# Optimization experiments

Hardware: AMD Instinct MI355X
Metric: run time of the kernel (lower is better)

## Reference

```python
import jax, jax.numpy as jnp
import numpy as np

B, N, S = 4, 4096, 1024
C1, C2, CO, K = 128, 256, 128, 16
BN_EPS = 1e-5


def setup_inputs() -> dict:
    key = jax.random.key(0)
    ks = jax.random.split(key, 8)
    s = 0.05
    return {
        "xyz1": jax.random.normal(ks[0], (B, N, 3), jnp.float32),
        "xyz2": jax.random.normal(ks[1], (B, S, 3), jnp.float32),
        "points1": jax.random.normal(ks[2], (B, C1, N), jnp.float32),
        "points2": jax.random.normal(ks[3], (B, C2, S), jnp.float32),
        # fuse = ConvBNReLU1D(384 -> 128, k=1)
        "fuse_w": jax.random.normal(ks[4], (CO, C1 + C2), jnp.float32) * s,
        "fuse_b": jnp.zeros((CO,), jnp.float32),
        "fuse_gamma": jnp.ones((CO,), jnp.float32),
        "fuse_beta": jnp.zeros((CO,), jnp.float32),
        # LaplacianUnit conv1x1 (128 -> 128) + BN
        "lu_w": jax.random.normal(ks[5], (CO, CO), jnp.float32) * s,
        "lu_b": jnp.zeros((CO,), jnp.float32),
        "lu_gamma": jnp.ones((CO,), jnp.float32),
        "lu_beta": jnp.zeros((CO,), jnp.float32),
    }


def _sqdist(a, b):
    # a: [B,N,3], b: [B,M,3] -> [B,N,M] squared euclidean distance
    return ((a * a).sum(-1)[:, :, None] + (b * b).sum(-1)[:, None, :]
            - 2.0 * jnp.einsum("bnc,bmc->bnm", a, b))


def _batchnorm1d(x, gamma, beta):
    # x: [B,C,N], training-mode BN (batch statistics, biased variance)
    mean = x.mean(axis=(0, 2), keepdims=True)
    var = ((x - mean) ** 2).mean(axis=(0, 2), keepdims=True)
    xn = (x - mean) * jax.lax.rsqrt(var + BN_EPS)
    return xn * gamma[None, :, None] + beta[None, :, None]


def _gather_points(pts, idx):
    # pts: [B,M,C], idx: [B,N,k] int -> [B,N,k,C]
    return jax.vmap(lambda p, i: p[i])(pts, idx)


def _forward(xyz1, xyz2, points1, points2,
             fuse_w, fuse_b, fuse_gamma, fuse_beta,
             lu_w, lu_b, lu_gamma, lu_beta):
    p2 = jnp.swapaxes(points2, 1, 2)  # [B,S,C2]
    # --- 3-point interpolation (note: torch code uses topk default largest=True) ---
    dists = _sqdist(xyz1, xyz2)                    # [B,N,S]
    top_d, idx = jax.lax.top_k(dists, 3)           # largest, descending (faithful)
    dist_recip = 1.0 / (top_d + 1e-8)
    weight = dist_recip / dist_recip.sum(axis=2, keepdims=True)  # [B,N,3]
    interp = (_gather_points(p2, idx) * weight[..., None]).sum(axis=2)  # [B,N,C2]
    # --- concat skip + fuse conv1x1 + BN + ReLU ---
    new_pts = jnp.concatenate([jnp.swapaxes(points1, 1, 2), interp], axis=-1)  # [B,N,C1+C2]
    x = jnp.einsum("oc,bnc->bon", fuse_w, new_pts) + fuse_b[None, :, None]     # [B,CO,N]
    x = jax.nn.relu(_batchnorm1d(x, fuse_gamma, fuse_beta))
    # --- LaplacianUnit: KNN(k=16) neighbor-sum minus self ---
    d_self = _sqdist(xyz1, xyz1)                   # [B,N,N]
    _, knn_idx = jax.lax.top_k(-d_self, K)         # k smallest distances -> [B,N,K]
    xt = jnp.swapaxes(x, 1, 2)                     # [B,N,CO]
    nbr_sum = _gather_points(xt, knn_idx).sum(axis=2)  # [B,N,CO]
    dx = jnp.swapaxes(nbr_sum, 1, 2) - x           # [B,CO,N]
    h = jnp.einsum("oc,bcn->bon", lu_w, dx) + lu_b[None, :, None]
    h = _batchnorm1d(jax.nn.relu(h), lu_gamma, lu_beta)  # bn(relu(conv(dx))), faithful order
    return x + h


def reference(xyz1, xyz2, points1, points2,
              fuse_w, fuse_b, fuse_gamma, fuse_beta,
              lu_w, lu_b, lu_gamma, lu_beta):
    return _forward(xyz1, xyz2, points1, points2,
                    fuse_w, fuse_b, fuse_gamma, fuse_beta,
                    lu_w, lu_b, lu_gamma, lu_beta)
```

## Files before the change

kernel.cpp:

```cpp
#include <hip/hip_runtime.h>
#include <cfloat>

#define NB 4
#define NN 4096
#define NS 1024
#define NC1 128
#define NC2 256
#define NCO 128
#define NCC 384
#define NK 16
#define KCHUNK 2048
#define KCAP 96
#define KPAD 97


__device__ __forceinline__ float norm3_np(float x, float y, float z) {
  return __fadd_rn(__fadd_rn(__fmul_rn(x, x), __fmul_rn(y, y)), __fmul_rn(z, z));
}

__device__ __forceinline__ float sqdist_np(float nq, float ns,
                                           float qx, float qy, float qz,
                                           float sx, float sy, float sz) {
  float dot = __fadd_rn(__fadd_rn(__fmul_rn(qx, sx), __fmul_rn(qy, sy)),
                        __fmul_rn(qz, sz));
  return __fsub_rn(__fadd_rn(nq, ns), __fmul_rn(2.0f, dot));
}

__global__ void transpose_k(const float* __restrict__ in, float* __restrict__ out,
                            int rows_in, int cols_in, long in_bs, long out_bs, int out_rs) {
  __shared__ float tile[32][33];
  const int b = blockIdx.z;
  const int c0 = blockIdx.x * 32, r0 = blockIdx.y * 32;
  const float* ib = in + (long)b * in_bs;
  float* ob = out + (long)b * out_bs;
#pragma unroll
  for (int k = 0; k < 32; k += 8) {
    tile[threadIdx.y + k][threadIdx.x] =
        ib[(long)(r0 + threadIdx.y + k) * cols_in + c0 + threadIdx.x];
  }
  __syncthreads();
#pragma unroll
  for (int k = 0; k < 32; k += 8) {
    ob[(long)(c0 + threadIdx.y + k) * out_rs + (r0 + threadIdx.x)] =
        tile[threadIdx.x][threadIdx.y + k];
  }
}

__global__ __launch_bounds__(256) void interp_top3_k(const float* __restrict__ xyz1,
                                                     const float* __restrict__ xyz2,
                                                     float* __restrict__ wW,
                                                     int* __restrict__ wIdx) {
  __shared__ float sx[NS], sy[NS], sz[NS], sn[NS];
  __shared__ float md[256 * 3];
  __shared__ int mi[256 * 3];
  const int b = blockIdx.y;
  const int tid = threadIdx.x;
  for (int i = tid; i < NS; i += 256) {
    long base = ((long)b * NS + i) * 3;
    float x = xyz2[base], y = xyz2[base + 1], z = xyz2[base + 2];
    sx[i] = x; sy[i] = y; sz[i] = z;
    sn[i] = norm3_np(x, y, z);
  }
  __syncthreads();
  const int q = (blockIdx.x << 5) + (tid >> 3);
  const int lane = tid & 7;
  long qb = ((long)b * NN + q) * 3;
  const float qx = xyz1[qb], qy = xyz1[qb + 1], qz = xyz1[qb + 2];
  const float nq = norm3_np(qx, qy, qz);
  float bd[3] = {-FLT_MAX, -FLT_MAX, -FLT_MAX};
  int bi[3] = {0x7fffffff, 0x7fffffff, 0x7fffffff};
  for (int s = lane; s < NS; s += 8) {
    float d = sqdist_np(nq, sn[s], qx, qy, qz, sx[s], sy[s], sz[s]);
    float cd = d; int ci = s;
#pragma unroll
    for (int j = 0; j < 3; ++j) {
      bool gt = cd > bd[j];
      float f = fmaxf(cd, bd[j]);
      float bk = fminf(cd, bd[j]);
      int fi = gt ? ci : bi[j];
      int ki = gt ? bi[j] : ci;
      bd[j] = f; bi[j] = fi; cd = bk; ci = ki;
    }
  }
#pragma unroll
  for (int j = 0; j < 3; ++j) { md[tid * 3 + j] = bd[j]; mi[tid * 3 + j] = bi[j]; }
  __syncthreads();
  if (lane == 0) {
    int p0 = 0, p1 = 0, p2 = 0, p3 = 0, p4 = 0, p5 = 0, p6 = 0, p7 = 0;
    float od[3]; int oi[3];
#pragma unroll
    for (int j = 0; j < 3; ++j) {
      float bv = -FLT_MAX; int bidx = 0x7fffffff; int bl = 0;
#define ITOP_CAND(l, pl)                                                     \
      {                                                                      \
        float t = (pl < 3) ? md[(tid + l) * 3 + pl] : -FLT_MAX;              \
        int ti = (pl < 3) ? mi[(tid + l) * 3 + pl] : 0x7fffffff;             \
        if (t > bv || (t == bv && ti < bidx)) { bv = t; bidx = ti; bl = l; } \
      }
      ITOP_CAND(0, p0) ITOP_CAND(1, p1) ITOP_CAND(2, p2) ITOP_CAND(3, p3)
      ITOP_CAND(4, p4) ITOP_CAND(5, p5) ITOP_CAND(6, p6) ITOP_CAND(7, p7)
#undef ITOP_CAND
      od[j] = bv; oi[j] = bidx;
      p0 += (bl == 0); p1 += (bl == 1); p2 += (bl == 2); p3 += (bl == 3);
      p4 += (bl == 4); p5 += (bl == 5); p6 += (bl == 6); p7 += (bl == 7);
    }
    float r0 = 1.f / (od[0] + 1e-8f);
    float r1 = 1.f / (od[1] + 1e-8f);
    float r2 = 1.f / (od[2] + 1e-8f);
    float sR = __fadd_rn(__fadd_rn(r0, r1), r2);
    long obase = ((long)b * NN + q) * 3;
    wW[obase + 0] = r0 / sR; wW[obase + 1] = r1 / sR; wW[obase + 2] = r2 / sR;
    wIdx[obase + 0] = oi[0]; wIdx[obase + 1] = oi[1]; wIdx[obase + 2] = oi[2];
  }
}

__global__ __launch_bounds__(256) void interp_fill_k(const float* __restrict__ p2t,
                                                     const float* __restrict__ wW,
                                                     const int* __restrict__ wIdx,
                                                     float* __restrict__ nt) {
  const int q = (blockIdx.x << 1) + (threadIdx.x >> 7);
  const int co = threadIdx.x & 127;
  const int b = q >> 12;
  long wb = (long)q * 3;
  float w0 = wW[wb], w1 = wW[wb + 1], w2 = wW[wb + 2];
  int i0 = wIdx[wb], i1 = wIdx[wb + 1], i2 = wIdx[wb + 2];
  const float* r0 = p2t + ((long)(b << 10) + i0) * NC2;
  const float* r1 = p2t + ((long)(b << 10) + i1) * NC2;
  const float* r2 = p2t + ((long)(b << 10) + i2) * NC2;
  float* orow = nt + (long)q * NCC + NC1;
#pragma unroll
  for (int h = 0; h < 2; ++h) {
    int c = co + 128 * h;
    orow[c] = w0 * r0[c] + w1 * r1[c] + w2 * r2[c];
  }
}

template <int C>
__global__ __launch_bounds__(256) void gemm_bias_k(const float* __restrict__ feat,
                                                   const float* __restrict__ W,
                                                   const float* __restrict__ bias,
                                                   float* __restrict__ out) {
  __shared__ float fL[64][36];
  __shared__ float wL[128][36];
  const int r0 = blockIdx.x * 64;
  const int tid = threadIdx.x;
  const int tn = tid & 15;
  const int to = tid >> 4;
  float acc[4][8];
#pragma unroll
  for (int i = 0; i < 4; ++i)
#pragma unroll
    for (int j = 0; j < 8; ++j) acc[i][j] = 0.f;

  for (int c0 = 0; c0 < C; c0 += 32) {
#pragma unroll
    for (int k = 0; k < 8; ++k) {
      int e = tid + 256 * k;
      int rr = e >> 5, cc = e & 31;
      fL[rr][cc] = feat[(long)(r0 + rr) * C + c0 + cc];
    }
#pragma unroll
    for (int k = 0; k < 16; ++k) {
      int e = tid + 256 * k;
      int rr = e >> 5, cc = e & 31;
      wL[rr][cc] = W[(long)rr * C + c0 + cc];
    }
    __syncthreads();
#pragma unroll
    for (int cc4 = 0; cc4 < 32; cc4 += 4) {
      float4 fv[4], wv[8];
#pragma unroll
      for (int i = 0; i < 4; ++i) fv[i] = *(const float4*)&fL[tn + 16 * i][cc4];
#pragma unroll
      for (int j = 0; j < 8; ++j) wv[j] = *(const float4*)&wL[to + 16 * j][cc4];
#pragma unroll
      for (int i = 0; i < 4; ++i)
#pragma unroll
        for (int j = 0; j < 8; ++j) {
          acc[i][j] += fv[i].x * wv[j].x + fv[i].y * wv[j].y +
                       fv[i].z * wv[j].z + fv[i].w * wv[j].w;
        }
    }
    __syncthreads();
  }
  const int b = r0 >> 12;
  const int n0 = r0 & 4095;
#pragma unroll
  for (int i = 0; i < 4; ++i) {
    int n = n0 + tn + 16 * i;
#pragma unroll
    for (int j = 0; j < 8; ++j) {
      int o = to + 16 * j;
      out[((long)(b * NCO + o) << 12) + n] = acc[i][j] + bias[o];
    }
  }
}

__global__ __launch_bounds__(256) void bn_stats_k(const float* __restrict__ v,
                                                  const float* __restrict__ gamma,
                                                  const float* __restrict__ beta,
                                                  float* __restrict__ stats, int relu_in) {
  __shared__ float rs[256], rq[256];
  const int o = blockIdx.x, tid = threadIdx.x;
  float s = 0.f;
  float vals_mean;
  for (int i = tid; i < NB * NN; i += 256) {
    int b = i >> 12, n = i & 4095;
    float val = v[(((long)b * NCO + o) << 12) + n];
    if (relu_in) val = fmaxf(val, 0.f);
    s += val;
  }
  rs[tid] = s;
  __syncthreads();
  for (int off = 128; off > 0; off >>= 1) {
    if (tid < off) rs[tid] += rs[tid + off];
    __syncthreads();
  }
  vals_mean = rs[0] * (1.f / 16384.f);
  float ss = 0.f;
  for (int i = tid; i < NB * NN; i += 256) {
    int b = i >> 12, n = i & 4095;
    float val = v[(((long)b * NCO + o) << 12) + n];
    if (relu_in) val = fmaxf(val, 0.f);
    float c = val - vals_mean;
    ss += c * c;
  }
  rq[tid] = ss;
  __syncthreads();
  for (int off = 128; off > 0; off >>= 1) {
    if (tid < off) rq[tid] += rq[tid + off];
    __syncthreads();
  }
  if (tid == 0) {
    float var = rq[0] * (1.f / 16384.f);
    float inv = rsqrtf(var + 1e-5f);
    stats[o] = vals_mean;
    stats[128 + o] = inv * gamma[o];
    stats[256 + o] = beta[o];
  }
}

__global__ void fuse_apply_k(const float* __restrict__ xp, const float* __restrict__ stats,
                             float* __restrict__ x, float* __restrict__ xt) {
  const int stride = gridDim.x * blockDim.x;
  for (int idx = blockIdx.x * blockDim.x + threadIdx.x; idx < NB * NCO * NN; idx += stride) {
    int o = (idx >> 12) & 127;
    int b = idx >> 19;
    int n = idx & 4095;
    float v = (xp[idx] - stats[o]) * stats[128 + o] + stats[256 + o];
    v = fmaxf(v, 0.f);
    x[idx] = v;
    xt[(((long)b << 12) + n) * NCO + o] = v;
  }
}

__global__ __launch_bounds__(256) void knn_k(const float* __restrict__ xyz1,
                                             int* __restrict__ knn) {
  __shared__ float4 sc[KCHUNK];
  __shared__ float bufd[32][KPAD];
  __shared__ int bufi[32][KPAD];
  const int b = blockIdx.y;
  const int tid = threadIdx.x;
  const int ql = tid >> 3;
  const int q = (blockIdx.x << 5) + ql;
  const int lane = tid & 7;
  const int gb = (tid & 63) - lane;
  const long qb = ((long)b * NN + q) * 3;
  const float qx = xyz1[qb], qy = xyz1[qb + 1], qz = xyz1[qb + 2];
  const float nq = norm3_np(qx, qy, qz);

  float a0 = FLT_MAX, a1 = FLT_MAX, c0 = FLT_MAX, c1 = FLT_MAX;
  for (int ch = 0; ch < 2; ++ch) {
    for (int i = tid; i < KCHUNK; i += 256) {
      long base = ((long)b * NN + ch * KCHUNK + i) * 3;
      float x = xyz1[base], y = xyz1[base + 1], z = xyz1[base + 2];
      sc[i] = make_float4(x, y, z, norm3_np(x, y, z));
    }
    __syncthreads();
#pragma unroll 2
    for (int i = lane; i < KCHUNK; i += 16) {
      float4 ca = sc[i];
      float4 cb = sc[i + 8];
      float da = sqdist_np(nq, ca.w, qx, qy, qz, ca.x, ca.y, ca.z);
      float db = sqdist_np(nq, cb.w, qx, qy, qz, cb.x, cb.y, cb.z);
      float ha = fmaxf(da, a0); a0 = fminf(da, a0); a1 = fminf(ha, a1);
      float hb = fmaxf(db, c0); c0 = fminf(db, c0); c1 = fminf(hb, c1);
    }
    __syncthreads();
  }
  float tau = fminf(fmaxf(a0, c0), fminf(a1, c1));
  tau = fmaxf(tau, __shfl_xor(tau, 1, 64));
  tau = fmaxf(tau, __shfl_xor(tau, 2, 64));
  tau = fmaxf(tau, __shfl_xor(tau, 4, 64));

  int mycnt = 0;
  for (int ch = 0; ch < 2; ++ch) {
    for (int i = tid; i < KCHUNK; i += 256) {
      long base = ((long)b * NN + ch * KCHUNK + i) * 3;
      float x = xyz1[base], y = xyz1[base + 1], z = xyz1[base + 2];
      sc[i] = make_float4(x, y, z, norm3_np(x, y, z));
    }
    __syncthreads();
    const int cb = ch * KCHUNK;
    for (int i = lane; i < KCHUNK; i += 8) {
      float4 cc = sc[i];
      float d = sqdist_np(nq, cc.w, qx, qy, qz, cc.x, cc.y, cc.z);
      bool surv = (d <= tau);
      unsigned long long m = __ballot(surv);
      unsigned gm = (unsigned)((m >> gb) & 0xFFull);
      if (surv) {
        int pos = mycnt + __popc(gm & ((1u << lane) - 1u));
        if (pos < KCAP) { bufd[ql][pos] = d; bufi[ql][pos] = cb + i; }
      }
      mycnt += __popc(gm);
    }
    __syncthreads();
  }

  float bd[NK]; int bi[NK];
#pragma unroll
  for (int j = 0; j < NK; ++j) { bd[j] = FLT_MAX; bi[j] = 0x7fffffff; }
  if (mycnt > KCAP) {
    for (int s = lane; s < NN; s += 8) {
      long base = ((long)b * NN + s) * 3;
      float x = xyz1[base], y = xyz1[base + 1], z = xyz1[base + 2];
      float d = sqdist_np(nq, norm3_np(x, y, z), qx, qy, qz, x, y, z);
      if (d <= tau) {
        float cd = d; int ci = s;
#pragma unroll
        for (int j = 0; j < NK; ++j) {
          bool lt = cd < bd[j];
          float dmin = fminf(cd, bd[j]);
          float dmax = fmaxf(cd, bd[j]);
          int imin = lt ? ci : bi[j];
          int imax = lt ? bi[j] : ci;
          bd[j] = dmin; bi[j] = imin; cd = dmax; ci = imax;
        }
      }
    }
  } else {
    for (int j0 = lane; j0 < mycnt; j0 += 8) {
      float cd = bufd[ql][j0]; int ci = bufi[ql][j0];
#pragma unroll
      for (int j = 0; j < NK; ++j) {
        bool lt = (cd < bd[j]) || (cd == bd[j] && ci < bi[j]);
        float nd = lt ? cd : bd[j];
        float xd = lt ? bd[j] : cd;
        int ni = lt ? ci : bi[j];
        int xi = lt ? bi[j] : ci;
        bd[j] = nd; bi[j] = ni; cd = xd; ci = xi;
      }
    }
  }
  __syncthreads();

  float* md = (float*)sc;
  int* mi = (int*)sc + 4096;
#pragma unroll
  for (int j = 0; j < NK; ++j) { md[tid * NK + j] = bd[j]; mi[tid * NK + j] = bi[j]; }
  __syncthreads();
  if (lane == 0) {
    int p0 = 0, p1 = 0, p2 = 0, p3 = 0, p4 = 0, p5 = 0, p6 = 0, p7 = 0;
    long obase = ((long)b * NN + q) * NK;
    for (int j = 0; j < NK; ++j) {
      float bv = FLT_MAX; int bidx = 0x7fffffff; int bl = 0;
#define KNN_CAND(l, pl)                                                      \
      {                                                                      \
        float t = (pl < NK) ? md[(tid + l) * NK + pl] : FLT_MAX;             \
        int ti = (pl < NK) ? mi[(tid + l) * NK + pl] : 0x7fffffff;           \
        if (t < bv || (t == bv && ti < bidx)) { bv = t; bidx = ti; bl = l; } \
      }
      KNN_CAND(0, p0) KNN_CAND(1, p1) KNN_CAND(2, p2) KNN_CAND(3, p3)
      KNN_CAND(4, p4) KNN_CAND(5, p5) KNN_CAND(6, p6) KNN_CAND(7, p7)
#undef KNN_CAND
      knn[obase + j] = bidx;
      p0 += (bl == 0); p1 += (bl == 1); p2 += (bl == 2); p3 += (bl == 3);
      p4 += (bl == 4); p5 += (bl == 5); p6 += (bl == 6); p7 += (bl == 7);
    }
  }
}

__global__ __launch_bounds__(256) void lap_gather_k(const float* __restrict__ xt,
                                                    const int* __restrict__ knn,
                                                    float* __restrict__ dxt) {
  const int q = (blockIdx.x << 1) + (threadIdx.x >> 7);
  const int o = threadIdx.x & 127;
  const int b = q >> 12;
  const int* kid = knn + (long)q * NK;
  const long bb = ((long)b << 12) * NCO;
  float s = 0.f;
#pragma unroll
  for (int k = 0; k < NK; ++k) {
    int m = kid[k];
    s += xt[bb + (long)m * NCO + o];
  }
  dxt[(long)q * NCO + o] = s - xt[(long)q * NCO + o];
}

__global__ void final_k(const float* __restrict__ x, const float* __restrict__ hp,
                        const float* __restrict__ stats, float* __restrict__ out) {
  const int stride = gridDim.x * blockDim.x;
  for (int idx = blockIdx.x * blockDim.x + threadIdx.x; idx < NB * NCO * NN; idx += stride) {
    int o = (idx >> 12) & 127;
    float r = fmaxf(hp[idx], 0.f);
    out[idx] = x[idx] + (r - stats[o]) * stats[128 + o] + stats[256 + o];
  }
}

extern "C" void kernel_launch(void* const* d_in, const int* in_sizes, int n_in,
                              void* d_out, int out_size, void* d_ws, size_t ws_size,
                              hipStream_t stream) {
  const float* xyz1 = (const float*)d_in[0];
  const float* xyz2 = (const float*)d_in[1];
  const float* points1 = (const float*)d_in[2];
  const float* points2 = (const float*)d_in[3];
  const float* fuse_w = (const float*)d_in[4];
  const float* fuse_b = (const float*)d_in[5];
  const float* fuse_g = (const float*)d_in[6];
  const float* fuse_be = (const float*)d_in[7];
  const float* lu_w = (const float*)d_in[8];
  const float* lu_b = (const float*)d_in[9];
  const float* lu_g = (const float*)d_in[10];
  const float* lu_be = (const float*)d_in[11];
  (void)in_sizes; (void)n_in; (void)out_size; (void)ws_size;

  char* ws = (char*)d_ws;
  float* p2t = (float*)(ws);
  float* wW = (float*)(ws + 4194304);
  int* wIdx = (int*)(ws + 4390912);
  float* st1 = (float*)(ws + 4587520);
  float* st2 = (float*)(ws + 4589056);
  int* knn = (int*)(ws + 4590592);
  float* nt = (float*)(ws + 5639168);
  float* xp = (float*)(ws + 30804992);
  float* x = (float*)(ws + 39193600);
  float* xt = nt;
  float* dxt = nt + 2097152;
  float* hp = nt + 4194304;

  dim3 tb(32, 8);
  transpose_k<<<dim3(32, 8, NB), tb, 0, stream>>>(points2, p2t, 256, 1024, 262144L, 262144L, 256);
  transpose_k<<<dim3(128, 4, NB), tb, 0, stream>>>(points1, nt, 128, 4096, 524288L, 1572864L, 384);
  interp_top3_k<<<dim3(128, NB), 256, 0, stream>>>(xyz1, xyz2, wW, wIdx);
  interp_fill_k<<<8192, 256, 0, stream>>>(p2t, wW, wIdx, nt);
  gemm_bias_k<NCC><<<256, 256, 0, stream>>>(nt, fuse_w, fuse_b, xp);
  bn_stats_k<<<128, 256, 0, stream>>>(xp, fuse_g, fuse_be, st1, 0);
  fuse_apply_k<<<2048, 256, 0, stream>>>(xp, st1, x, xt);
  knn_k<<<dim3(128, NB), 256, 0, stream>>>(xyz1, knn);
  lap_gather_k<<<8192, 256, 0, stream>>>(xt, knn, dxt);
  gemm_bias_k<NCO><<<256, 256, 0, stream>>>(dxt, lu_w, lu_b, hp);
  bn_stats_k<<<128, 256, 0, stream>>>(hp, lu_g, lu_be, st2, 1);
  final_k<<<2048, 256, 0, stream>>>(x, hp, st2, (float*)d_out);
}
```

Measured before the change: 303.1 us.

## Restructure KNN kernel to 16 lanes per query with redundant per-lane top-K selection

The KNN kernel now assigns 16 lanes per query (16 queries per block, twice the blocks) instead of 8, with smaller shared-memory chunks and a larger survivor buffer. In the threshold pass each lane keeps its two smallest distances and a shuffle butterfly combines them into tau. In the selection phase every lane redundantly insertion-sorts the whole survivor list, so the shared-memory 8-way merge and its extra barriers go away; lane j then writes the j-th neighbour. This adds parallelism and removes the serial merge, at the cost of 16x redundant sorting work per query and a fully serial overflow fallback over all N points.

Result: slower. 682.1 us (+125.1%).

```diff
diff --git a/kernel.cpp b/kernel.cpp
--- a/kernel.cpp
+++ b/kernel.cpp
@@ -9,9 +9,9 @@
 #define NCO 128
 #define NCC 384
 #define NK 16
-#define KCHUNK 2048
-#define KCAP 96
-#define KPAD 97
+#define KCHUNK 1024
+#define KCAP 128
+#define KPAD 129
 
 
 __device__ __forceinline__ float norm3_np(float x, float y, float z) {
@@ -257,44 +257,44 @@
 __global__ __launch_bounds__(256) void knn_k(const float* __restrict__ xyz1,
                                              int* __restrict__ knn) {
   __shared__ float4 sc[KCHUNK];
-  __shared__ float bufd[32][KPAD];
-  __shared__ int bufi[32][KPAD];
+  __shared__ float bufd[16][KPAD];
+  __shared__ int bufi[16][KPAD];
   const int b = blockIdx.y;
   const int tid = threadIdx.x;
-  const int ql = tid >> 3;
-  const int q = (blockIdx.x << 5) + ql;
-  const int lane = tid & 7;
+  const int ql = tid >> 4;
+  const int q = (blockIdx.x << 4) + ql;
+  const int lane = tid & 15;
   const int gb = (tid & 63) - lane;
   const long qb = ((long)b * NN + q) * 3;
   const float qx = xyz1[qb], qy = xyz1[qb + 1], qz = xyz1[qb + 2];
   const float nq = norm3_np(qx, qy, qz);
 
-  float a0 = FLT_MAX, a1 = FLT_MAX, c0 = FLT_MAX, c1 = FLT_MAX;
-  for (int ch = 0; ch < 2; ++ch) {
+  float t0 = FLT_MAX, t1 = FLT_MAX;
+  for (int ch = 0; ch < 4; ++ch) {
     for (int i = tid; i < KCHUNK; i += 256) {
       long base = ((long)b * NN + ch * KCHUNK + i) * 3;
       float x = xyz1[base], y = xyz1[base + 1], z = xyz1[base + 2];
       sc[i] = make_float4(x, y, z, norm3_np(x, y, z));
     }
     __syncthreads();
-#pragma unroll 2
     for (int i = lane; i < KCHUNK; i += 16) {
-      float4 ca = sc[i];
-      float4 cb = sc[i + 8];
-      float da = sqdist_np(nq, ca.w, qx, qy, qz, ca.x, ca.y, ca.z);
-      float db = sqdist_np(nq, cb.w, qx, qy, qz, cb.x, cb.y, cb.z);
-      float ha = fmaxf(da, a0); a0 = fminf(da, a0); a1 = fminf(ha, a1);
-      float hb = fmaxf(db, c0); c0 = fminf(db, c0); c1 = fminf(hb, c1);
-    }
-    __syncthreads();
-  }
-  float tau = fminf(fmaxf(a0, c0), fminf(a1, c1));
-  tau = fmaxf(tau, __shfl_xor(tau, 1, 64));
+      float4 cc = sc[i];
+      float d = sqdist_np(nq, cc.w, qx, qy, qz, cc.x, cc.y, cc.z);
+      float hi = fmaxf(d, t0);
+      t0 = fminf(d, t0);
+      t1 = fminf(hi, t1);
+    }
+    __syncthreads();
+  }
+  float p0 = __shfl_xor(t0, 1, 64);
+  float p1 = __shfl_xor(t1, 1, 64);
+  float tau = fminf(fmaxf(t0, p0), fminf(t1, p1));
   tau = fmaxf(tau, __shfl_xor(tau, 2, 64));
   tau = fmaxf(tau, __shfl_xor(tau, 4, 64));
+  tau = fmaxf(tau, __shfl_xor(tau, 8, 64));
 
   int mycnt = 0;
-  for (int ch = 0; ch < 2; ++ch) {
+  for (int ch = 0; ch < 4; ++ch) {
     for (int i = tid; i < KCHUNK; i += 256) {
       long base = ((long)b * NN + ch * KCHUNK + i) * 3;
       float x = xyz1[base], y = xyz1[base + 1], z = xyz1[base + 2];
@@ -302,12 +302,12 @@
     }
     __syncthreads();
     const int cb = ch * KCHUNK;
-    for (int i = lane; i < KCHUNK; i += 8) {
+    for (int i = lane; i < KCHUNK; i += 16) {
       float4 cc = sc[i];
       float d = sqdist_np(nq, cc.w, qx, qy, qz, cc.x, cc.y, cc.z);
       bool surv = (d <= tau);
       unsigned long long m = __ballot(surv);
-      unsigned gm = (unsigned)((m >> gb) & 0xFFull);
+      unsigned gm = (unsigned)((m >> gb) & 0xFFFFull);
       if (surv) {
         int pos = mycnt + __popc(gm & ((1u << lane) - 1u));
         if (pos < KCAP) { bufd[ql][pos] = d; bufi[ql][pos] = cb + i; }
@@ -321,7 +321,7 @@
 #pragma unroll
   for (int j = 0; j < NK; ++j) { bd[j] = FLT_MAX; bi[j] = 0x7fffffff; }
   if (mycnt > KCAP) {
-    for (int s = lane; s < NN; s += 8) {
+    for (int s = 0; s < NN; ++s) {
       long base = ((long)b * NN + s) * 3;
       float x = xyz1[base], y = xyz1[base + 1], z = xyz1[base + 2];
       float d = sqdist_np(nq, norm3_np(x, y, z), qx, qy, qz, x, y, z);
@@ -339,7 +339,7 @@
       }
     }
   } else {
-    for (int j0 = lane; j0 < mycnt; j0 += 8) {
+    for (int j0 = 0; j0 < mycnt; ++j0) {
       float cd = bufd[ql][j0]; int ci = bufi[ql][j0];
 #pragma unroll
       for (int j = 0; j < NK; ++j) {
@@ -352,31 +352,10 @@
       }
     }
   }
-  __syncthreads();
-
-  float* md = (float*)sc;
-  int* mi = (int*)sc + 4096;
-#pragma unroll
-  for (int j = 0; j < NK; ++j) { md[tid * NK + j] = bd[j]; mi[tid * NK + j] = bi[j]; }
-  __syncthreads();
-  if (lane == 0) {
-    int p0 = 0, p1 = 0, p2 = 0, p3 = 0, p4 = 0, p5 = 0, p6 = 0, p7 = 0;
-    long obase = ((long)b * NN + q) * NK;
-    for (int j = 0; j < NK; ++j) {
-      float bv = FLT_MAX; int bidx = 0x7fffffff; int bl = 0;
-#define KNN_CAND(l, pl)                                                      \
-      {                                                                      \
-        float t = (pl < NK) ? md[(tid + l) * NK + pl] : FLT_MAX;             \
-        int ti = (pl < NK) ? mi[(tid + l) * NK + pl] : 0x7fffffff;           \
-        if (t < bv || (t == bv && ti < bidx)) { bv = t; bidx = ti; bl = l; } \
-      }
-      KNN_CAND(0, p0) KNN_CAND(1, p1) KNN_CAND(2, p2) KNN_CAND(3, p3)
-      KNN_CAND(4, p4) KNN_CAND(5, p5) KNN_CAND(6, p6) KNN_CAND(7, p7)
-#undef KNN_CAND
-      knn[obase + j] = bidx;
-      p0 += (bl == 0); p1 += (bl == 1); p2 += (bl == 2); p3 += (bl == 3);
-      p4 += (bl == 4); p5 += (bl == 5); p6 += (bl == 6); p7 += (bl == 7);
-    }
+  const long obase = ((long)b * NN + q) * NK;
+#pragma unroll
+  for (int j = 0; j < NK; ++j) {
+    if (lane == j) knn[obase + j] = bi[j];
   }
 }
 
@@ -446,7 +425,7 @@
   gemm_bias_k<NCC><<<256, 256, 0, stream>>>(nt, fuse_w, fuse_b, xp);
   bn_stats_k<<<128, 256, 0, stream>>>(xp, fuse_g, fuse_be, st1, 0);
   fuse_apply_k<<<2048, 256, 0, stream>>>(xp, st1, x, xt);
-  knn_k<<<dim3(128, NB), 256, 0, stream>>>(xyz1, knn);
+  knn_k<<<dim3(256, NB), 256, 0, stream>>>(xyz1, knn);
   lap_gather_k<<<8192, 256, 0, stream>>>(xt, knn, dxt);
   gemm_bias_k<NCO><<<256, 256, 0, stream>>>(dxt, lu_w, lu_b, hp);
   bn_stats_k<<<128, 256, 0, stream>>>(hp, lu_g, lu_be, st2, 1);
```
